# Kernel optimization log

Hardware: AMD Instinct MI355X
Metric: run time of the kernel (lower is better)

The kernel has to match this reference:

```python
import jax, jax.numpy as jnp
import numpy as np

EPS = 1e-5
HEADS, DK, DV = 8, 32, 32


def conv3x3(x, w, b):
    # regular (non-depthwise, despite the name) 3x3 conv, stride 1, padding 1
    y = jax.lax.conv_general_dilated(
        x, w, window_strides=(1, 1), padding='SAME',
        dimension_numbers=('NCHW', 'OIHW', 'NCHW'))
    return y + b[None, :, None, None]


def setup_inputs() -> dict:
    key = jax.random.key(0)
    ks = jax.random.split(key, 16)
    C = 256
    d = {}
    d['x'] = jax.random.normal(ks[0], (8, C, 32, 32), jnp.float32)
    s_lin = 1.0 / np.sqrt(C)
    s_conv = 1.0 / np.sqrt(C * 9)
    d['Wq'] = jax.random.normal(ks[1], (C, HEADS * DK), jnp.float32) * s_lin
    d['bq'] = jnp.zeros((HEADS * DK,), jnp.float32)
    d['conv_k_w'] = jax.random.normal(ks[2], (C, C, 3, 3), jnp.float32) * s_conv
    d['conv_k_b'] = jnp.zeros((C,), jnp.float32)
    d['Wk'] = jax.random.normal(ks[3], (C, HEADS * DK), jnp.float32) * s_lin
    d['bk'] = jnp.zeros((HEADS * DK,), jnp.float32)
    d['conv_v_w'] = jax.random.normal(ks[4], (C, C, 3, 3), jnp.float32) * s_conv
    d['conv_v_b'] = jnp.zeros((C,), jnp.float32)
    d['Wv'] = jax.random.normal(ks[5], (C, HEADS * DV), jnp.float32) * s_lin
    d['bv'] = jnp.zeros((HEADS * DV,), jnp.float32)
    d['Wo'] = jax.random.normal(ks[6], (HEADS * DV, C), jnp.float32) * s_lin
    d['bo'] = jnp.zeros((C,), jnp.float32)
    d['B'] = jax.random.normal(ks[7], (1, HEADS, 1024, 1024), jnp.float32) * 0.02
    return d


def reference(x, Wq, bq, conv_k_w, conv_k_b, Wk, bk, conv_v_w, conv_v_b, Wv, bv, Wo, bo, B):
    b, c, h, w = x.shape
    hw = h * w
    xr = x.reshape(b, c, hw).transpose(0, 2, 1)  # [b, hw, c]
    # F.layer_norm with normalized_shape == full shape: whole-tensor stats, no affine
    m = jnp.mean(xr)
    v = jnp.mean((xr - m) ** 2)
    xn = (xr - m) * jax.lax.rsqrt(v + EPS)

    q = (xn @ Wq + bq).reshape(b, hw, HEADS, DK).transpose(0, 2, 1, 3)  # [b,H,hw,dk]

    k = conv3x3(x, conv_k_w, conv_k_b)  # stride 1 -> same spatial size (per source)
    k = k.reshape(b, c, hw).transpose(0, 2, 1)
    k = (k @ Wk + bk).reshape(b, hw, HEADS, DK).transpose(0, 2, 1, 3)

    vv = conv3x3(x, conv_v_w, conv_v_b)
    vv = vv.reshape(b, c, hw).transpose(0, 2, 1)
    vv = (vv @ Wv + bv).reshape(b, hw, HEADS, DV).transpose(0, 2, 1, 3)

    scale = DK ** (-0.5)
    attn = jnp.einsum('bhid,bhjd->bhij', q, k) * scale + B  # [b,H,hw,hw]
    attn = jax.nn.softmax(attn, axis=-1)
    out = jnp.einsum('bhij,bhjd->bhid', attn, vv)  # [b,H,hw,dv]
    out = out.transpose(0, 2, 1, 3).reshape(b, hw, HEADS * DV)
    out = out @ Wo + bo  # [b, hw, c]
    # faithful to torch .view(b, c, h, w): raw reshape, NO transpose
    out = out.reshape(b, c, h, w)
    return out + x
```

## Files before the change

### kernel.cpp

```cpp
#include <hip/hip_runtime.h>
#include <hip/hip_bf16.h>
#include <math.h>

#define B_     8
#define C_     256
#define HW_    1024
#define NTOT   (B_*C_*HW_)
#define HEADS_ 8
#define DK_    32
#define SCALE_ 0.17677669529663687f

#define F_STATS 0
#define F_PART  16
#define F_YK2   8192
#define F_YV2   (F_YK2 + NTOT)
#define F_XB    (F_YV2 + NTOT)
#define F_WT    (F_XB + NTOT/2)
#define F_QB    (F_WT + 589824)
#define F_KB    (F_QB + NTOT/2)
#define F_VT    (F_KB + NTOT/2)

typedef float f32x4 __attribute__((ext_vector_type(4)));
typedef short short8 __attribute__((ext_vector_type(8)));

__device__ __forceinline__ short bf16s(float f) {
    __hip_bfloat16 h = __float2bfloat16(f);
    return *(short*)&h;
}
__device__ __forceinline__ unsigned pack_bf16(float a, float b) {
    unsigned ua = (unsigned short)bf16s(a);
    unsigned ub = (unsigned short)bf16s(b);
    return ua | (ub << 16);
}
__device__ __forceinline__ void gload_lds16(const short* g, short* l) {
    __builtin_amdgcn_global_load_lds(
        (const __attribute__((address_space(1))) unsigned*)g,
        (__attribute__((address_space(3))) unsigned*)l, 16, 0, 0);
}

__global__ void k_prep_x(const float* __restrict__ x, short* __restrict__ xb,
                         float* __restrict__ part) {
    __shared__ short t[64 * 258];
    __shared__ float ls[4], ls2[4];
    int b = blockIdx.x >> 4, p0 = (blockIdx.x & 15) << 6;
    int tid = threadIdx.x;
    float s = 0.f, s2 = 0.f;
    for (int i = tid; i < 256 * 64; i += 256) {
        int ci = i >> 6, p = i & 63;
        float v = x[(b * C_ + ci) * HW_ + p0 + p];
        s += v; s2 += v * v;
        t[p * 258 + ci] = bf16s(v);
    }
    for (int o = 32; o; o >>= 1) { s += __shfl_down(s, o); s2 += __shfl_down(s2, o); }
    int wid = tid >> 6, lane = tid & 63;
    if (lane == 0) { ls[wid] = s; ls2[wid] = s2; }
    __syncthreads();
    if (tid == 0) {
        float a = 0.f, bb = 0.f;
        for (int i = 0; i < 4; i++) { a += ls[i]; bb += ls2[i]; }
        part[blockIdx.x * 2] = a; part[blockIdx.x * 2 + 1] = bb;
    }
    for (int i = tid; i < 64 * 256; i += 256) {
        int p = i >> 8, ci = i & 255;
        xb[(b * HW_ + p0 + p) * C_ + ci] = t[p * 258 + ci];
    }
}

__global__ void k_stats(const float* __restrict__ part, float* __restrict__ stats) {
    __shared__ float ls[256], ls2[256];
    float s = 0.f, s2 = 0.f;
    for (int i = threadIdx.x; i < 128; i += 256) { s += part[2 * i]; s2 += part[2 * i + 1]; }
    ls[threadIdx.x] = s; ls2[threadIdx.x] = s2;
    __syncthreads();
    for (int off = 128; off; off >>= 1) {
        if (threadIdx.x < off) { ls[threadIdx.x] += ls[threadIdx.x + off]; ls2[threadIdx.x] += ls2[threadIdx.x + off]; }
        __syncthreads();
    }
    if (threadIdx.x == 0) {
        float m = ls[0] / (float)NTOT;
        float var = ls2[0] / (float)NTOT - m * m;
        stats[0] = m;
        stats[1] = rsqrtf(var + 1e-5f);
    }
}

__global__ void k_prep_w(const float* __restrict__ wk, const float* __restrict__ wv,
                         short* __restrict__ wt) {
    int idx = blockIdx.x * 256 + threadIdx.x;
    int ci0 = (idx << 2) & 255;
    int rest = idx >> 6;
    int n = rest & 511, tap = rest >> 9;
    const float* src = (n < 256) ? (wk + (n * C_) * 9) : (wv + ((n - 256) * C_) * 9);
    short4 o;
    short* op = (short*)&o;
    for (int u = 0; u < 4; u++)
        op[u] = bf16s(src[(ci0 + u) * 9 + tap]);
    *(short4*)&wt[((tap * 512 + n) * C_) + ci0] = o;
}

__global__ void k_prep_pw(const float* __restrict__ Wq, const float* __restrict__ Wk,
                          const float* __restrict__ Wv, const float* __restrict__ Wo,
                          short* __restrict__ wt4) {
    __shared__ short t[64 * 66];
    int mi = blockIdx.x >> 4, tl = blockIdx.x & 15;
    int c0 = (tl >> 2) * 64, e0 = (tl & 3) * 64;
    const float* W = mi == 0 ? Wq : mi == 1 ? Wk : mi == 2 ? Wv : Wo;
    int tid = threadIdx.x;
    for (int i = tid; i < 4096; i += 256) {
        int cl = i >> 6, el = i & 63;
        t[cl * 66 + el] = bf16s(W[(c0 + cl) * 256 + e0 + el]);
    }
    __syncthreads();
    for (int i = tid; i < 4096; i += 256) {
        int el = i >> 6, cl = i & 63;
        wt4[mi * 65536 + (e0 + el) * 256 + c0 + cl] = t[cl * 66 + el];
    }
}

__global__ void k_prep_beta(const float* __restrict__ Wq, const float* __restrict__ bq,
                            const float* __restrict__ stats, float* __restrict__ beta0) {
    __shared__ float ps[1024];
    int t = threadIdx.x, e = t & 255, part = t >> 8;
    float s = 0.f;
    for (int c = part * 64; c < part * 64 + 64; c++) s += Wq[c * 256 + e];
    ps[t] = s;
    __syncthreads();
    if (t < 256) {
        float cs = ps[t] + ps[t + 256] + ps[t + 512] + ps[t + 768];
        beta0[t] = (bq[t] - stats[0] * stats[1] * cs) * SCALE_;
    }
}

__device__ __forceinline__ int a_off(int slot, int chunk) {
    int c = chunk ^ (slot & 3);
    int s = slot ^ ((slot >> 2) & 1);
    return s * 64 + c * 16;
}

__global__ __launch_bounds__(512, 4)
void k_conv_mfma(const short* __restrict__ xb, const short* __restrict__ wt,
                 const float* __restrict__ bk, const float* __restrict__ bv,
                 float* __restrict__ yk2, float* __restrict__ yv2) {
    __shared__ short a_sh[204 * 32];
    __shared__ short b_sh[9 * 2048];
    int bid = blockIdx.x;
    int nt = bid & 7, pt = (bid >> 3) & 7, b = bid >> 6;
    int R0 = pt * 4;
    int tid = threadIdx.x;
    int w = tid >> 6, l = tid & 63;
    int wm = w >> 1, wn = w & 1;
    int col16 = l & 15, kq = l >> 4;

    int offs[2], loffs[2];
    #pragma unroll
    for (int it = 0; it < 2; it++) {
        int i = tid + it * 512;
        if (i < 816) {
            int slot = i >> 2, chunk = i & 3;
            int ty = slot / 34, tx = slot - ty * 34;
            int Y = R0 - 1 + ty, X = tx - 1;
            offs[it] = ((unsigned)Y < 32u && (unsigned)X < 32u)
                       ? ((b * HW_ + Y * 32 + X) * C_ + chunk * 8) : -1;
            loffs[it] = a_off(slot, chunk);
        } else { offs[it] = -1; loffs[it] = -1; }
    }

    int bgoff[5];
    int nbj = 0;
    #pragma unroll 1
    for (int j = w; j < 36; j += 8) {
        int S = j * 64 + l;
        int tap = S >> 8, s = S & 255;
        int colb = s >> 2, kqs = s & 3;
        int kq2 = kqs ^ ((colb >> 1) & 3);
        bgoff[nbj++] = (tap * 512 + nt * 64 + colb) * C_ + kq2 * 8;
    }

    f32x4 acc[2][2];
    #pragma unroll
    for (int m = 0; m < 2; m++)
        #pragma unroll
        for (int n = 0; n < 2; n++) acc[m][n] = (f32x4)0.f;

    int sr[2];
    #pragma unroll
    for (int nf = 0; nf < 2; nf++) {
        int colb = wn * 32 + nf * 16 + col16;
        sr[nf] = (colb << 2) | (kq ^ ((colb >> 1) & 3));
    }

    {
        short8 sv[2];
        #pragma unroll
        for (int it = 0; it < 2; it++)
            sv[it] = (offs[it] >= 0) ? *(const short8*)(xb + offs[it]) : (short8)0;
        int jj = 0;
        #pragma unroll 1
        for (int j = w; j < 36; j += 8, jj++)
            gload_lds16(wt + bgoff[jj], b_sh + j * 512);
        #pragma unroll
        for (int it = 0; it < 2; it++)
            if (loffs[it] >= 0) *(short8*)((char*)a_sh + loffs[it]) = sv[it];
    }
    __syncthreads();

    #pragma unroll 1
    for (int step = 0; step < 8; step++) {
        const char* ab = (const char*)a_sh;
        const char* bbp = (const char*)b_sh;
        #pragma unroll
        for (int tap = 0; tap < 9; tap++) {
            const int dyi = tap / 3, dxi = tap % 3;
            short8 af[2], bf[2];
            #pragma unroll
            for (int mf = 0; mf < 2; mf++) {
                int slot = (wm + dyi) * 34 + mf * 16 + col16 + dxi;
                af[mf] = *(const short8*)(ab + a_off(slot, kq));
            }
            #pragma unroll
            for (int nf = 0; nf < 2; nf++)
                bf[nf] = *(const short8*)(bbp + tap * 4096 + sr[nf] * 16);
            #pragma unroll
            for (int mf = 0; mf < 2; mf++)
                #pragma unroll
                for (int nf = 0; nf < 2; nf++)
                    acc[mf][nf] = __builtin_amdgcn_mfma_f32_16x16x32_bf16(af[mf], bf[nf], acc[mf][nf], 0, 0, 0);
        }
        if (step < 7) {
            int ci0n = step * 32 + 32;
            __syncthreads();
            short8 sv[2];
            #pragma unroll
            for (int it = 0; it < 2; it++)
                sv[it] = (offs[it] >= 0) ? *(const short8*)(xb + offs[it] + ci0n) : (short8)0;
            int jj = 0;
            #pragma unroll 1
            for (int j = w; j < 36; j += 8, jj++)
                gload_lds16(wt + bgoff[jj] + ci0n, b_sh + j * 512);
            #pragma unroll
            for (int it = 0; it < 2; it++)
                if (loffs[it] >= 0) *(short8*)((char*)a_sh + loffs[it]) = sv[it];
            __syncthreads();
        }
    }

    const bool isv = (nt >= 4);
    float* dst = isv ? yv2 : yk2;
    const float* bias = isv ? bv : bk;
    int cbase = (nt & 3) * 64 + wn * 32 + col16;
    #pragma unroll
    for (int nf = 0; nf < 2; nf++) {
        int co = cbase + nf * 16;
        float bi = bias[co];
        #pragma unroll
        for (int mf = 0; mf < 2; mf++) {
            #pragma unroll
            for (int r = 0; r < 4; r++) {
                int pixel = pt * 128 + wm * 32 + mf * 16 + kq * 4 + r;
                dst[(b * HW_ + pixel) * C_ + co] = acc[mf][nf][r] + bi;
            }
        }
    }
}

__global__ void k_proj_mfma(const short* __restrict__ xb,
                            const float* __restrict__ yk2, const float* __restrict__ yv2,
                            const short* __restrict__ wt4,
                            const float* __restrict__ bkp, const float* __restrict__ bvp,
                            const float* __restrict__ stats, const float* __restrict__ beta0,
                            short* __restrict__ qb, short* __restrict__ kb,
                            short* __restrict__ vt) {
    __shared__ char smem[17408];
    int pj = blockIdx.x, pt = blockIdx.y, b = blockIdx.z;
    int p0 = pt * 32;
    int tid = threadIdx.x, w = tid >> 6, l = tid & 63;
    int c16 = l & 15, kq = l >> 4;

    if (pj == 0) {
        #pragma unroll
        for (int it = 0; it < 4; it++) {
            int i = it * 256 + tid;
            int slab = i >> 7, rem = i & 127, slot = rem >> 2, chunk = rem & 3;
            short8 v = *(const short8*)(xb + ((b * HW_ + p0 + slot) * C_ + slab * 32 + chunk * 8));
            *(short8*)(smem + slab * 2048 + a_off(slot, chunk)) = v;
        }
    } else {
        const float* src = (pj == 1) ? yk2 : yv2;
        #pragma unroll
        for (int it = 0; it < 4; it++) {
            int i = it * 256 + tid;
            int slab = i >> 7, rem = i & 127, slot = rem >> 2, chunk = rem & 3;
            const float* sp = src + (b * HW_ + p0 + slot) * C_ + slab * 32 + chunk * 8;
            float4 f0 = *(const float4*)sp;
            float4 f1 = *(const float4*)(sp + 4);
            short8 v;
            v[0] = bf16s(f0.x); v[1] = bf16s(f0.y); v[2] = bf16s(f0.z); v[3] = bf16s(f0.w);
            v[4] = bf16s(f1.x); v[5] = bf16s(f1.y); v[6] = bf16s(f1.z); v[7] = bf16s(f1.w);
            *(short8*)(smem + slab * 2048 + a_off(slot, chunk)) = v;
        }
    }
    __syncthreads();

    const short* wt_p = wt4 + pj * 65536;
    f32x4 acc[2][4];
    #pragma unroll
    for (int m = 0; m < 2; m++)
        #pragma unroll
        for (int n = 0; n < 4; n++) acc[m][n] = (f32x4)0.f;

    for (int s = 0; s < 8; s++) {
        short8 af[2], bf[4];
        #pragma unroll
        for (int mf = 0; mf < 2; mf++)
            af[mf] = *(const short8*)(smem + s * 2048 + a_off(mf * 16 + c16, kq));
        #pragma unroll
        for (int nf = 0; nf < 4; nf++)
            bf[nf] = *(const short8*)(wt_p + (w * 64 + nf * 16 + c16) * 256 + s * 32 + kq * 8);
        #pragma unroll
        for (int mf = 0; mf < 2; mf++)
            #pragma unroll
            for (int nf = 0; nf < 4; nf++)
                acc[mf][nf] = __builtin_amdgcn_mfma_f32_16x16x32_bf16(af[mf], bf[nf], acc[mf][nf], 0, 0, 0);
    }

    float alpha = (pj == 0) ? stats[1] * SCALE_ : 1.f;
    float beta[4];
    #pragma unroll
    for (int nf = 0; nf < 4; nf++) {
        int e = w * 64 + nf * 16 + c16;
        beta[nf] = (pj == 0) ? beta0[e] : (pj == 1 ? bkp[e] : bvp[e]);
    }
    __syncthreads();

    short* rp = (short*)smem + w * 2176;
    if (pj < 2) {
        #pragma unroll
        for (int mf = 0; mf < 2; mf++)
            #pragma unroll
            for (int nf = 0; nf < 4; nf++)
                #pragma unroll
                for (int rg = 0; rg < 4; rg++) {
                    int px = mf * 16 + kq * 4 + rg, el = nf * 16 + c16;
                    rp[px * 66 + el] = bf16s(alpha * acc[mf][nf][rg] + beta[nf]);
                }
        __syncthreads();
        short* dst = (pj == 0) ? qb : kb;
        #pragma unroll
        for (int j = 0; j < 4; j++) {
            int px = j * 8 + (l >> 3), el = (l & 7) * 8;
            short8 v = *(const short8*)(rp + px * 66 + el);
            int e = w * 64 + el, h = e >> 5, d = e & 31;
            *(short8*)(dst + ((b * 8 + h) * HW_ + p0 + px) * DK_ + d) = v;
        }
    } else {
        #pragma unroll
        for (int mf = 0; mf < 2; mf++)
            #pragma unroll
            for (int nf = 0; nf < 4; nf++)
                #pragma unroll
                for (int rg = 0; rg < 4; rg++) {
                    int px = mf * 16 + kq * 4 + rg, el = nf * 16 + c16;
                    rp[el * 34 + px] = bf16s(acc[mf][nf][rg] + beta[nf]);
                }
        __syncthreads();
        #pragma unroll
        for (int j = 0; j < 4; j++) {
            int el = j * 16 + (l >> 2), px = (l & 3) * 8;
            short8 v = *(const short8*)(rp + el * 34 + px);
            int e = w * 64 + el, h = e >> 5, d = e & 31;
            *(short8*)(vt + ((b * 8 + h) * DK_ + d) * HW_ + p0 + px) = v;
        }
    }
}

__global__ void k_attn(const short* __restrict__ qb, const short* __restrict__ kb,
                       const short* __restrict__ vt, const float* __restrict__ Bb,
                       short* __restrict__ ao) {
    __shared__ __align__(16) short Qs[64 * 32];
    __shared__ __align__(16) short Ks[64 * 32];
    __shared__ __align__(16) short Vs[32 * 64];
    __shared__ __align__(16) short Ps[4][16 * 64];
    int bid = blockIdx.x;
    int h = bid & 7, b = (bid >> 3) & 7, qt = bid >> 6;
    int bh = b * HEADS_ + h;
    int tid = threadIdx.x, w = tid >> 6, l = tid & 63;
    int g = l >> 4, c16 = l & 15;

    *(short8*)(Qs + tid * 8) = *(const short8*)(qb + (bh * HW_ + qt * 64) * DK_ + tid * 8);

    const float* Brow = Bb + (h * HW_ + qt * 64 + w * 16 + c16) * HW_;
    float m_run = -1e30f, l_run = 0.f;
    f32x4 ot[2];
    ot[0] = (f32x4)0.f; ot[1] = (f32x4)0.f;
    char* pbase = (char*)&Ps[w][0];
    int vrow = tid >> 3, vch = tid & 7;

    for (int kv0 = 0; kv0 < HW_; kv0 += 64) {
        __syncthreads();
        *(short8*)(Ks + tid * 8) = *(const short8*)(kb + (bh * HW_ + kv0) * DK_ + tid * 8);
        {
            short8 v = *(const short8*)(vt + (bh * DK_ + vrow) * HW_ + kv0 + vch * 8);
            *(short8*)((char*)Vs + vrow * 128 + ((vch * 16) ^ ((vrow & 7) << 4))) = v;
        }
        __syncthreads();

        short8 qf = *(const short8*)(Qs + (w * 16 + c16) * DK_ + g * 8);
        f32x4 st[4];
        #pragma unroll
        for (int mt = 0; mt < 4; mt++) {
            float4 bi = *(const float4*)(Brow + kv0 + mt * 16 + g * 4);
            f32x4 acc; acc[0] = bi.x; acc[1] = bi.y; acc[2] = bi.z; acc[3] = bi.w;
            short8 kf = *(const short8*)(Ks + (mt * 16 + c16) * DK_ + g * 8);
            st[mt] = __builtin_amdgcn_mfma_f32_16x16x32_bf16(kf, qf, acc, 0, 0, 0);
        }

        float mx = m_run;
        #pragma unroll
        for (int mt = 0; mt < 4; mt++)
            #pragma unroll
            for (int rg = 0; rg < 4; rg++) mx = fmaxf(mx, st[mt][rg]);
        mx = fmaxf(mx, __shfl_xor(mx, 16));
        mx = fmaxf(mx, __shfl_xor(mx, 32));
        float f = __expf(m_run - mx);
        m_run = mx;
        float s = 0.f;
        #pragma unroll
        for (int mt = 0; mt < 4; mt++)
            #pragma unroll
            for (int rg = 0; rg < 4; rg++) {
                float e_ = __expf(st[mt][rg] - mx);
                st[mt][rg] = e_;
                s += e_;
            }
        s += __shfl_xor(s, 16);
        s += __shfl_xor(s, 32);
        l_run = l_run * f + s;

        int fv = __float_as_int(f);
        #pragma unroll
        for (int rg = 0; rg < 4; rg++) {
            float fr = __int_as_float(__builtin_amdgcn_ds_bpermute((g * 4 + rg) << 2, fv));
            ot[0][rg] *= fr;
            ot[1][rg] *= fr;
        }

        #pragma unroll
        for (int mt = 0; mt < 4; mt++) {
            unsigned lo = pack_bf16(st[mt][0], st[mt][1]);
            unsigned hi = pack_bf16(st[mt][2], st[mt][3]);
            unsigned long long pr = (unsigned long long)lo | ((unsigned long long)hi << 32);
            *(unsigned long long*)(pbase + c16 * 128 + ((mt * 32 + g * 8) ^ ((c16 & 7) << 4))) = pr;
        }
        #pragma unroll
        for (int kt = 0; kt < 2; kt++) {
            short8 pf = *(const short8*)(pbase + c16 * 128 + ((kt * 64 + g * 16) ^ ((c16 & 7) << 4)));
            #pragma unroll
            for (int nt = 0; nt < 2; nt++) {
                short8 vf = *(const short8*)((char*)Vs + (c16 + 16 * nt) * 128 + ((kt * 64 + g * 16) ^ ((c16 & 7) << 4)));
                ot[nt] = __builtin_amdgcn_mfma_f32_16x16x32_bf16(pf, vf, ot[nt], 0, 0, 0);
            }
        }
    }

    float linv = 1.f / l_run;
    int lrv = __float_as_int(linv);
    #pragma unroll
    for (int rg = 0; rg < 4; rg++) {
        float li = __int_as_float(__builtin_amdgcn_ds_bpermute((g * 4 + rg) << 2, lrv));
        int qg = qt * 64 + w * 16 + g * 4 + rg;
        #pragma unroll
        for (int nt = 0; nt < 2; nt++)
            ao[(b * HW_ + qg) * C_ + h * DK_ + nt * 16 + c16] = bf16s(ot[nt][rg] * li);
    }
}

__global__ void k_out_mfma(const short* __restrict__ aob, const short* __restrict__ wot,
                           const float* __restrict__ bo, const float* __restrict__ x,
                           float* __restrict__ out) {
    __shared__ char smem[16384];
    int pt = blockIdx.x, b = blockIdx.y;
    int p0 = pt * 32;
    int tid = threadIdx.x, w = tid >> 6, l = tid & 63;
    int c16 = l & 15, kq = l >> 4;

    #pragma unroll
    for (int it = 0; it < 4; it++) {
        int i = it * 256 + tid;
        int slab = i >> 7, rem = i & 127, slot = rem >> 2, chunk = rem & 3;
        short8 v = *(const short8*)(aob + ((b * HW_ + p0 + slot) * C_ + slab * 32 + chunk * 8));
        *(short8*)(smem + slab * 2048 + a_off(slot, chunk)) = v;
    }
    __syncthreads();

    f32x4 acc[2][4];
    #pragma unroll
    for (int m = 0; m < 2; m++)
        #pragma unroll
        for (int n = 0; n < 4; n++) acc[m][n] = (f32x4)0.f;

    for (int s = 0; s < 8; s++) {
        short8 af[2], bf[4];
        #pragma unroll
        for (int mf = 0; mf < 2; mf++)
            af[mf] = *(const short8*)(smem + s * 2048 + a_off(mf * 16 + c16, kq));
        #pragma unroll
        for (int nf = 0; nf < 4; nf++)
            bf[nf] = *(const short8*)(wot + (w * 64 + nf * 16 + c16) * 256 + s * 32 + kq * 8);
        #pragma unroll
        for (int mf = 0; mf < 2; mf++)
            #pragma unroll
            for (int nf = 0; nf < 4; nf++)
                acc[mf][nf] = __builtin_amdgcn_mfma_f32_16x16x32_bf16(af[mf], bf[nf], acc[mf][nf], 0, 0, 0);
    }

    #pragma unroll
    for (int nf = 0; nf < 4; nf++) {
        int e = w * 64 + nf * 16 + c16;
        float bov = bo[e];
        #pragma unroll
        for (int mf = 0; mf < 2; mf++) {
            #pragma unroll
            for (int rg = 0; rg < 4; rg++) {
                int px = mf * 16 + kq * 4 + rg;
                int idx = b * (C_ * HW_) + (p0 + px) * 256 + e;
                out[idx] = acc[mf][nf][rg] + bov + x[idx];
            }
        }
    }
}

extern "C" void kernel_launch(void* const* d_in, const int* in_sizes, int n_in,
                              void* d_out, int out_size, void* d_ws, size_t ws_size,
                              hipStream_t stream) {
    const float* x   = (const float*)d_in[0];
    const float* Wq  = (const float*)d_in[1];
    const float* bq  = (const float*)d_in[2];
    const float* ckw = (const float*)d_in[3];
    const float* ckb = (const float*)d_in[4];
    const float* Wk  = (const float*)d_in[5];
    const float* bk  = (const float*)d_in[6];
    const float* cvw = (const float*)d_in[7];
    const float* cvb = (const float*)d_in[8];
    const float* Wv  = (const float*)d_in[9];
    const float* bv  = (const float*)d_in[10];
    const float* Wo  = (const float*)d_in[11];
    const float* bo  = (const float*)d_in[12];
    const float* Bb  = (const float*)d_in[13];
    float* ws  = (float*)d_ws;
    float* out = (float*)d_out;

    short* xb      = (short*)(ws + F_XB);
    short* wt      = (short*)(ws + F_WT);
    short* wt4     = (short*)(ws + F_WT);
    float* beta0   = ws + F_WT + 131072;
    short* qb      = (short*)(ws + F_QB);
    short* kb      = (short*)(ws + F_KB);
    short* vt      = (short*)(ws + F_VT);
    short* aob     = (short*)(ws + F_YK2);
    short* wot     = wt4 + 3 * 65536;

    k_prep_x   <<<128,  256, 0, stream>>>(x, xb, ws + F_PART);
    k_stats    <<<1,    256, 0, stream>>>(ws + F_PART, ws + F_STATS);
    k_prep_w   <<<1152, 256, 0, stream>>>(ckw, cvw, wt);
    k_conv_mfma<<<512,  512, 0, stream>>>(xb, wt, ckb, cvb, ws + F_YK2, ws + F_YV2);
    k_prep_pw  <<<64,   256, 0, stream>>>(Wq, Wk, Wv, Wo, wt4);
    k_prep_beta<<<1,   1024, 0, stream>>>(Wq, bq, ws + F_STATS, beta0);
    k_proj_mfma<<<dim3(3, 32, 8), 256, 0, stream>>>(xb, ws + F_YK2, ws + F_YV2,
                                                    wt4, bk, bv, ws + F_STATS, beta0,
                                                    qb, kb, vt);
    k_attn     <<<1024, 256, 0, stream>>>(qb, kb, vt, Bb, aob);
    k_out_mfma <<<dim3(32, 8), 256, 0, stream>>>(aob, wot, bo, x, out);
}
```

Measured before the change: 144.3 us.

## Double KV tile, register-prefetch next tile, lazy softmax rescale in attention

The attention kernel now processes 128 keys per iteration instead of 64 and prefetches the next K/V tile into registers while the current tile is computed. Q is loaded straight into registers rather than staged through shared memory. The online-softmax rescale is skipped unless the running max grows by more than a threshold of 8, and s_setprio hints bracket the MFMA phases. The aim is to hide global load latency and cut per-iteration sync and exp overhead, at the cost of more registers and LDS, plus a numerical risk if exp values exceed the threshold headroom.

Result: no change. 145.9 us (+1.1%).

```diff
diff --git a/kernel.cpp b/kernel.cpp
--- a/kernel.cpp
+++ b/kernel.cpp
@@ -373,93 +373,114 @@
     }
 }
 
-__global__ void k_attn(const short* __restrict__ qb, const short* __restrict__ kb,
-                       const short* __restrict__ vt, const float* __restrict__ Bb,
-                       short* __restrict__ ao) {
-    __shared__ __align__(16) short Qs[64 * 32];
-    __shared__ __align__(16) short Ks[64 * 32];
-    __shared__ __align__(16) short Vs[32 * 64];
-    __shared__ __align__(16) short Ps[4][16 * 64];
+__global__ __launch_bounds__(256, 4)
+void k_attn(const short* __restrict__ qb, const short* __restrict__ kb,
+            const short* __restrict__ vt, const float* __restrict__ Bb,
+            short* __restrict__ ao) {
+    __shared__ __align__(16) short Ks[128 * 32];
+    __shared__ __align__(16) short Vs[32 * 128];
+    __shared__ __align__(16) short Ps[4][16 * 128];
     int bid = blockIdx.x;
     int h = bid & 7, b = (bid >> 3) & 7, qt = bid >> 6;
     int bh = b * HEADS_ + h;
     int tid = threadIdx.x, w = tid >> 6, l = tid & 63;
     int g = l >> 4, c16 = l & 15;
 
-    *(short8*)(Qs + tid * 8) = *(const short8*)(qb + (bh * HW_ + qt * 64) * DK_ + tid * 8);
-
-    const float* Brow = Bb + (h * HW_ + qt * 64 + w * 16 + c16) * HW_;
+    int qrow = qt * 64 + w * 16 + c16;
+    short8 qf = *(const short8*)(qb + (bh * HW_ + qrow) * DK_ + g * 8);
+
+    const float* Brow = Bb + (h * HW_ + qrow) * HW_;
     float m_run = -1e30f, l_run = 0.f;
     f32x4 ot[2];
     ot[0] = (f32x4)0.f; ot[1] = (f32x4)0.f;
     char* pbase = (char*)&Ps[w][0];
-    int vrow = tid >> 3, vch = tid & 7;
-
-    for (int kv0 = 0; kv0 < HW_; kv0 += 64) {
+
+    int vrow = tid >> 4, vch = tid & 15;
+    int vrow2 = (tid + 256) >> 4, vch2 = (tid + 256) & 15;
+
+    short8 kreg[2], vreg[2];
+    kreg[0] = *(const short8*)(kb + (bh * HW_) * DK_ + tid * 8);
+    kreg[1] = *(const short8*)(kb + (bh * HW_) * DK_ + (tid + 256) * 8);
+    vreg[0] = *(const short8*)(vt + (bh * DK_ + vrow) * HW_ + vch * 8);
+    vreg[1] = *(const short8*)(vt + (bh * DK_ + vrow2) * HW_ + vch2 * 8);
+
+    for (int kv0 = 0; kv0 < HW_; kv0 += 128) {
         __syncthreads();
-        *(short8*)(Ks + tid * 8) = *(const short8*)(kb + (bh * HW_ + kv0) * DK_ + tid * 8);
-        {
-            short8 v = *(const short8*)(vt + (bh * DK_ + vrow) * HW_ + kv0 + vch * 8);
-            *(short8*)((char*)Vs + vrow * 128 + ((vch * 16) ^ ((vrow & 7) << 4))) = v;
-        }
+        *(short8*)(Ks + tid * 8) = kreg[0];
+        *(short8*)(Ks + (tid + 256) * 8) = kreg[1];
+        *(short8*)((char*)Vs + vrow * 256 + ((vch * 16) ^ ((vrow & 7) << 4))) = vreg[0];
+        *(short8*)((char*)Vs + vrow2 * 256 + ((vch2 * 16) ^ ((vrow2 & 7) << 4))) = vreg[1];
         __syncthreads();
-
-        short8 qf = *(const short8*)(Qs + (w * 16 + c16) * DK_ + g * 8);
-        f32x4 st[4];
-        #pragma unroll
-        for (int mt = 0; mt < 4; mt++) {
+        if (kv0 + 128 < HW_) {
+            int nk = kv0 + 128;
+            kreg[0] = *(const short8*)(kb + (bh * HW_ + nk) * DK_ + tid * 8);
+            kreg[1] = *(const short8*)(kb + (bh * HW_ + nk) * DK_ + (tid + 256) * 8);
+            vreg[0] = *(const short8*)(vt + (bh * DK_ + vrow) * HW_ + nk + vch * 8);
+            vreg[1] = *(const short8*)(vt + (bh * DK_ + vrow2) * HW_ + nk + vch2 * 8);
+        }
+
+        f32x4 st[8];
+        __builtin_amdgcn_s_setprio(1);
+        #pragma unroll
+        for (int mt = 0; mt < 8; mt++) {
             float4 bi = *(const float4*)(Brow + kv0 + mt * 16 + g * 4);
             f32x4 acc; acc[0] = bi.x; acc[1] = bi.y; acc[2] = bi.z; acc[3] = bi.w;
             short8 kf = *(const short8*)(Ks + (mt * 16 + c16) * DK_ + g * 8);
             st[mt] = __builtin_amdgcn_mfma_f32_16x16x32_bf16(kf, qf, acc, 0, 0, 0);
         }
-
-        float mx = m_run;
-        #pragma unroll
-        for (int mt = 0; mt < 4; mt++)
-            #pragma unroll
-            for (int rg = 0; rg < 4; rg++) mx = fmaxf(mx, st[mt][rg]);
-        mx = fmaxf(mx, __shfl_xor(mx, 16));
-        mx = fmaxf(mx, __shfl_xor(mx, 32));
-        float f = __expf(m_run - mx);
-        m_run = mx;
+        __builtin_amdgcn_s_setprio(0);
+
+        float pmax = st[0][0];
+        #pragma unroll
+        for (int mt = 0; mt < 8; mt++)
+            #pragma unroll
+            for (int rg = 0; rg < 4; rg++) pmax = fmaxf(pmax, st[mt][rg]);
+        pmax = fmaxf(pmax, __shfl_xor(pmax, 16));
+        pmax = fmaxf(pmax, __shfl_xor(pmax, 32));
+        if (!__all(pmax <= m_run + 8.f)) {
+            float mnew = fmaxf(m_run, pmax);
+            float f = __expf(m_run - mnew);
+            m_run = mnew;
+            l_run *= f;
+            int fv = __float_as_int(f);
+            #pragma unroll
+            for (int rg = 0; rg < 4; rg++) {
+                float fr = __int_as_float(__builtin_amdgcn_ds_bpermute((g * 4 + rg) << 2, fv));
+                ot[0][rg] *= fr;
+                ot[1][rg] *= fr;
+            }
+        }
         float s = 0.f;
         #pragma unroll
-        for (int mt = 0; mt < 4; mt++)
+        for (int mt = 0; mt < 8; mt++)
             #pragma unroll
             for (int rg = 0; rg < 4; rg++) {
-                float e_ = __expf(st[mt][rg] - mx);
+                float e_ = __expf(st[mt][rg] - m_run);
                 st[mt][rg] = e_;
                 s += e_;
             }
         s += __shfl_xor(s, 16);
         s += __shfl_xor(s, 32);
-        l_run = l_run * f + s;
-
-        int fv = __float_as_int(f);
-        #pragma unroll
-        for (int rg = 0; rg < 4; rg++) {
-            float fr = __int_as_float(__builtin_amdgcn_ds_bpermute((g * 4 + rg) << 2, fv));
-            ot[0][rg] *= fr;
-            ot[1][rg] *= fr;
-        }
-
-        #pragma unroll
-        for (int mt = 0; mt < 4; mt++) {
+        l_run += s;
+
+        #pragma unroll
+        for (int mt = 0; mt < 8; mt++) {
             unsigned lo = pack_bf16(st[mt][0], st[mt][1]);
             unsigned hi = pack_bf16(st[mt][2], st[mt][3]);
             unsigned long long pr = (unsigned long long)lo | ((unsigned long long)hi << 32);
-            *(unsigned long long*)(pbase + c16 * 128 + ((mt * 32 + g * 8) ^ ((c16 & 7) << 4))) = pr;
-        }
-        #pragma unroll
-        for (int kt = 0; kt < 2; kt++) {
-            short8 pf = *(const short8*)(pbase + c16 * 128 + ((kt * 64 + g * 16) ^ ((c16 & 7) << 4)));
+            *(unsigned long long*)(pbase + c16 * 256 + ((mt * 32 + g * 8) ^ ((c16 & 7) << 4))) = pr;
+        }
+        __builtin_amdgcn_s_setprio(1);
+        #pragma unroll
+        for (int kt = 0; kt < 4; kt++) {
+            short8 pf = *(const short8*)(pbase + c16 * 256 + ((kt * 64 + g * 16) ^ ((c16 & 7) << 4)));
             #pragma unroll
             for (int nt = 0; nt < 2; nt++) {
-                short8 vf = *(const short8*)((char*)Vs + (c16 + 16 * nt) * 128 + ((kt * 64 + g * 16) ^ ((c16 & 7) << 4)));
+                short8 vf = *(const short8*)((char*)Vs + (c16 + 16 * nt) * 256 + ((kt * 64 + g * 16) ^ ((c16 & 7) << 4)));
                 ot[nt] = __builtin_amdgcn_mfma_f32_16x16x32_bf16(pf, vf, ot[nt], 0, 0, 0);
             }
         }
+        __builtin_amdgcn_s_setprio(0);
     }
 
     float linv = 1.f / l_run;
```
